# Kernel optimization log

Measured on AMD Instinct MI355X. Metric: run time of the kernel, lower is better.

The kernel has to match this reference:

```python
import jax, jax.numpy as jnp
import numpy as np

N_NODES = 100000
N_EDGES = 600000
N_REL = 4
N_HEADS = 4
DIM = 128  # in_dim == out_dim (required by out = zeros_like(x) + index_add_ of out_dim msgs)
HEAD_DIM = DIM // N_HEADS
NEG_SLOPE = 0.2


def setup_inputs() -> dict:
    key = jax.random.key(0)
    k1, k2, k3, k4, k5 = jax.random.split(key, 5)
    x = jax.random.normal(k1, (N_NODES, DIM), dtype=jnp.float32)
    edge_index = jax.random.randint(k2, (2, N_EDGES), 0, N_NODES, dtype=jnp.int64)
    edge_types = jax.random.randint(k3, (N_EDGES,), 0, N_REL, dtype=jnp.int64)
    # per-relation linear weights, xavier-ish scale
    W = jax.random.normal(k4, (N_REL, DIM, DIM), dtype=jnp.float32) * (1.0 / np.sqrt(DIM))
    # attention vectors [R, H, 2*head_dim]
    attn = jax.random.normal(k5, (N_REL, N_HEADS, 2 * HEAD_DIM), dtype=jnp.float32) * 0.1
    return {"x": x, "edge_index": edge_index, "edge_types": edge_types, "W": W, "attn": attn}


def reference(x, edge_index, edge_types, W, attn):
    N = x.shape[0]
    R, H, twoD = attn.shape
    D = twoD // 2
    E = edge_types.shape[0]

    # per-relation linear transform: [R, N, H, D]
    x_rel = jnp.einsum('ni,rio->rno', x, W).reshape(R, N, H, D)

    src, dst = edge_index[0], edge_index[1]

    # gather per-edge features with the edge's relation
    src_feat = x_rel[edge_types, src]            # [E, H, D]
    dst_feat = x_rel[edge_types, dst]            # [E, H, D]
    a = attn[edge_types]                         # [E, H, 2D]

    # attention logits + LeakyReLU(0.2)
    cat = jnp.concatenate([src_feat, dst_feat], axis=-1)  # [E, H, 2D]
    alpha = jnp.sum(cat * a, axis=-1)                     # [E, H]
    alpha = jnp.where(alpha > 0, alpha, NEG_SLOPE * alpha)

    # segment softmax over edges sharing (relation, dst)
    seg = edge_types * N + dst                            # [E]
    S = R * N
    m = jax.ops.segment_max(alpha, seg, num_segments=S)   # [S, H]
    alpha_exp = jnp.exp(alpha - m[seg])
    denom = jax.ops.segment_sum(alpha_exp, seg, num_segments=S)
    w = alpha_exp / denom[seg]                            # [E, H]

    # weighted messages, scatter-add to dst
    msg = (src_feat * w[..., None]).reshape(E, H * D)     # [E, out_dim]
    out = jax.ops.segment_sum(msg, dst, num_segments=N)   # [N, out_dim]
    return out
```

## Files before the change

### kernel.cpp

```cpp
#include <hip/hip_runtime.h>
#include <hip/hip_bf16.h>
#include <stdint.h>

#define N_NODES 100000
#define N_EDGES 600000
#define N_REL 4
#define N_HEADS 4
#define DIM 128
#define HEAD_DIM 32
#define NEG_SLOPE 0.2f

typedef unsigned int uint;
typedef unsigned short ushort;
typedef __attribute__((ext_vector_type(8))) short bf16x8;
typedef __attribute__((ext_vector_type(4))) float f32x4;

__device__ __forceinline__ float bf2f(ushort u) { return __uint_as_float(((uint)u) << 16); }
__device__ __forceinline__ float lo2f(uint u) { return __uint_as_float(u << 16); }
__device__ __forceinline__ float hi2f(uint u) { return __uint_as_float(u & 0xffff0000u); }
__device__ __forceinline__ ushort f2bf(float f) {
    uint u = __float_as_uint(f);
    uint r = (u + 0x7fffu + ((u >> 16) & 1u)) >> 16;
    return (ushort)r;
}
__device__ __forceinline__ float lrelu(float v) { return v > 0.f ? v : NEG_SLOPE * v; }

__device__ __forceinline__ int bf16_plaus(ushort u) {
    int ex = (u >> 7) & 0xFF;
    return (ex >= 100 && ex <= 140) ? 1 : 0;
}
__global__ void k_detect(const ushort* __restrict__ x, const ushort* __restrict__ W,
                         const ushort* __restrict__ attn, const int* __restrict__ ei,
                         const int* __restrict__ et, int* __restrict__ flags) {
    __shared__ int cnt[5];
    int t = threadIdx.x;
    if (t < 5) cnt[t] = 0;
    __syncthreads();
    if (t < 128) {
        atomicAdd(&cnt[0], bf16_plaus(x[2 * t]));
        atomicAdd(&cnt[1], bf16_plaus(W[2 * t]));
        atomicAdd(&cnt[2], bf16_plaus(attn[2 * t]));
        atomicAdd(&cnt[3], (ei[2 * t + 1] != 0) ? 1 : 0);
        atomicAdd(&cnt[4], (et[2 * t + 1] != 0) ? 1 : 0);
    }
    __syncthreads();
    if (t == 0) {
        flags[0] = (cnt[0] < 64) ? 1 : 0;
        flags[1] = (cnt[1] < 64) ? 1 : 0;
        flags[2] = (cnt[2] < 64) ? 1 : 0;
        flags[3] = (cnt[3] < 8) ? 1 : 0;
        flags[4] = (cnt[4] < 8) ? 1 : 0;
    }
}

__global__ __launch_bounds__(256) void k_canon_i(
    const int* __restrict__ src, int* __restrict__ dst, int n,
    const int* __restrict__ flags, int flagIdx) {
    int i0 = (blockIdx.x * 256 + threadIdx.x) * 4;
    int i64f = flags[flagIdx];
#pragma unroll
    for (int j = 0; j < 4; j++) {
        int i = i0 + j;
        if (i < n) dst[i] = i64f ? src[2 * i] : src[i];
    }
}

__global__ __launch_bounds__(256) void k_cvt_x(
    const void* __restrict__ xv, const int* __restrict__ flags,
    ushort* __restrict__ x_bf)
{
    int t = blockIdx.x * 256 + threadIdx.x;
    if (t >= N_NODES * DIM / 8) return;
    if (flags[0]) {
        const float4* p = (const float4*)xv + (size_t)t * 2;
        float4 f0 = p[0], f1 = p[1];
        uint4 o;
        o.x = (uint)f2bf(f0.x) | ((uint)f2bf(f0.y) << 16);
        o.y = (uint)f2bf(f0.z) | ((uint)f2bf(f0.w) << 16);
        o.z = (uint)f2bf(f1.x) | ((uint)f2bf(f1.y) << 16);
        o.w = (uint)f2bf(f1.z) | ((uint)f2bf(f1.w) << 16);
        ((uint4*)x_bf)[t] = o;
    } else {
        ((uint4*)x_bf)[t] = ((const uint4*)xv)[t];
    }
}

__global__ __launch_bounds__(256) void k_prep_w(
    const void* __restrict__ Wv, const void* __restrict__ av,
    const int* __restrict__ flags,
    ushort* __restrict__ Wt_g, ushort* __restrict__ at_g)
{
    __shared__ ushort wt[128][136];
    const int r = blockIdx.x;
    const int tid = threadIdx.x;
    const int wf = flags[1], af = flags[2];

    if (wf) {
        const float4* Wg = (const float4*)((const float*)Wv + (size_t)r * DIM * DIM);
        for (int it = 0; it < 16; ++it) {
            int idx = tid + it * 256;
            int k = idx >> 5, n4 = (idx & 31) * 4;
            float4 v = Wg[idx];
            wt[n4 + 0][k] = f2bf(v.x);
            wt[n4 + 1][k] = f2bf(v.y);
            wt[n4 + 2][k] = f2bf(v.z);
            wt[n4 + 3][k] = f2bf(v.w);
        }
    } else {
        const ushort* Wg = (const ushort*)Wv + (size_t)r * DIM * DIM;
        for (int it = 0; it < 16; ++it) {
            int idx = tid + it * 256;
            int k = idx >> 5, n4 = (idx & 31) * 4;
            const ushort* p = Wg + (size_t)k * DIM + n4;
            wt[n4 + 0][k] = p[0];
            wt[n4 + 1][k] = p[1];
            wt[n4 + 2][k] = p[2];
            wt[n4 + 3][k] = p[3];
        }
    }
    __syncthreads();

    for (int it = 0; it < 9; ++it) {
        int idx = tid + it * 256;
        if (idx < 2176) {
            int row = idx / 17, c8 = (idx % 17) * 8;
            *(uint4*)(Wt_g + ((size_t)r * 128 + row) * 136 + c8) = *(const uint4*)&wt[row][c8];
        }
    }
    for (int it = 0; it < 9; ++it) {
        int idx = tid + it * 256;
        if (idx < 16 * 136) {
            int n = idx / 136, k = idx % 136;
            int h = n & 3, sd = (n >> 2) & 1;
            float v = 0.f;
            if (n < 8 && k < 128) {
                int d = k - h * 32;
                if (d >= 0 && d < 32) {
                    size_t ai = ((size_t)(r * N_HEADS + h)) * 64 + (size_t)sd * 32 + d;
                    v = af ? ((const float*)av)[ai] : bf2f(((const ushort*)av)[ai]);
                }
            }
            at_g[((size_t)r * 16 + n) * 136 + k] = f2bf(v);
        }
    }
}

__global__ __launch_bounds__(256) void k_gemm_mfma(
    const ushort* __restrict__ x_bf, const ushort* __restrict__ Wt_g,
    const ushort* __restrict__ at_g,
    ushort* __restrict__ x_rel, float* __restrict__ sTab)
{
    __shared__ ushort wt[128][136];
    __shared__ ushort at[16][136];

    const int tid = threadIdx.x;
    const int wave = tid >> 6, lane = tid & 63;
    const int quad = lane >> 4, l16 = lane & 15;
    const int r = blockIdx.x & 3;
    const int n0 = (blockIdx.x >> 2) * 128;

    {
        const uint4* src  = (const uint4*)(Wt_g + (size_t)r * 128 * 136);
        const uint4* srcA = (const uint4*)(at_g + (size_t)r * 16 * 136);
        uint4* dstL = (uint4*)&wt[0][0];
        uint4* dstA = (uint4*)&at[0][0];
#pragma unroll
        for (int it = 0; it < 10; ++it) {
            int idx = tid + it * 256;
            if (idx < 2176) dstL[idx] = src[idx];
            else if (idx < 2448) dstA[idx - 2176] = srcA[idx - 2176];
        }
    }

    const int rowA0 = n0 + wave * 32 + l16;
    const int rowA1 = rowA0 + 16;
    const size_t rA0 = (size_t)min(rowA0, N_NODES - 1) * DIM;
    const size_t rA1 = (size_t)min(rowA1, N_NODES - 1) * DIM;

    __syncthreads();

    f32x4 acc[2][8];
#pragma unroll
    for (int rt = 0; rt < 2; ++rt)
#pragma unroll
        for (int ct = 0; ct < 8; ++ct) acc[rt][ct] = (f32x4){0.f, 0.f, 0.f, 0.f};

#pragma unroll
    for (int q = 0; q < 4; ++q) {
        const int kb = q * 32 + quad * 8;
        bf16x8 a0 = *(const bf16x8*)(x_bf + rA0 + kb);
        bf16x8 a1 = *(const bf16x8*)(x_bf + rA1 + kb);
#pragma unroll
        for (int ct = 0; ct < 8; ++ct) {
            bf16x8 b = *(const bf16x8*)&wt[ct * 16 + l16][kb];
            acc[0][ct] = __builtin_amdgcn_mfma_f32_16x16x32_bf16(a0, b, acc[0][ct], 0, 0, 0);
            acc[1][ct] = __builtin_amdgcn_mfma_f32_16x16x32_bf16(a1, b, acc[1][ct], 0, 0, 0);
        }
    }
    __syncthreads();

    {
        ushort* rp = &wt[0][0];
#pragma unroll
        for (int rt = 0; rt < 2; ++rt) {
            int rowb = wave * 32 + rt * 16 + quad * 4;
#pragma unroll
            for (int ct = 0; ct < 8; ++ct) {
                int col = ct * 16 + l16;
#pragma unroll
                for (int reg = 0; reg < 4; ++reg)
                    rp[(rowb + reg) * 136 + col] = f2bf(acc[rt][ct][reg]);
            }
        }
    }
    __syncthreads();

    {
        const ushort* rp = &wt[0][0];
        f32x4 sacc[2];
        sacc[0] = (f32x4){0.f, 0.f, 0.f, 0.f};
        sacc[1] = (f32x4){0.f, 0.f, 0.f, 0.f};
#pragma unroll
        for (int q = 0; q < 4; ++q) {
            const int kb = q * 32 + quad * 8;
            bf16x8 a0 = *(const bf16x8*)(rp + (wave * 32 + l16) * 136 + kb);
            bf16x8 a1 = *(const bf16x8*)(rp + (wave * 32 + 16 + l16) * 136 + kb);
            bf16x8 bat = *(const bf16x8*)&at[l16][kb];
            sacc[0] = __builtin_amdgcn_mfma_f32_16x16x32_bf16(a0, bat, sacc[0], 0, 0, 0);
            sacc[1] = __builtin_amdgcn_mfma_f32_16x16x32_bf16(a1, bat, sacc[1], 0, 0, 0);
        }
        if (l16 < 8) {
#pragma unroll
            for (int rt = 0; rt < 2; ++rt) {
#pragma unroll
                for (int reg = 0; reg < 4; ++reg) {
                    int node = n0 + wave * 32 + rt * 16 + quad * 4 + reg;
                    if (node < N_NODES)
                        sTab[((size_t)r * N_NODES + node) * 8 + l16] = sacc[rt][reg];
                }
            }
        }
    }

    {
        const ushort* rp = &wt[0][0];
        const size_t rbase = (size_t)r * N_NODES * DIM;
#pragma unroll
        for (int p = 0; p < 8; ++p) {
            int row = p * 16 + (tid >> 4);
            int chunk = tid & 15;
            int node = n0 + row;
            if (node < N_NODES) {
                uint4 v = *(const uint4*)(rp + row * 136 + chunk * 8);
                *(uint4*)(x_rel + rbase + (size_t)node * DIM + chunk * 8) = v;
            }
        }
    }
}

__global__ __launch_bounds__(256) void k_hist(
    const int* __restrict__ ei, uint* __restrict__ deg)
{
    int e = blockIdx.x * 256 + threadIdx.x;
    if (e >= N_EDGES) return;
    atomicAdd(&deg[ei[N_EDGES + e]], 1u);
}

__global__ __launch_bounds__(256) void k_scan1(
    const uint* __restrict__ deg, uint* __restrict__ excl, uint* __restrict__ bsum)
{
    __shared__ uint tmp[256];
    int i = blockIdx.x * 256 + threadIdx.x;
    uint v = (i < N_NODES) ? deg[i] : 0u;
    tmp[threadIdx.x] = v;
    __syncthreads();
    for (int off = 1; off < 256; off <<= 1) {
        uint t = (threadIdx.x >= off) ? tmp[threadIdx.x - off] : 0u;
        __syncthreads();
        tmp[threadIdx.x] += t;
        __syncthreads();
    }
    if (i < N_NODES) excl[i] = tmp[threadIdx.x] - v;
    if (threadIdx.x == 255) bsum[blockIdx.x] = tmp[255];
}

__global__ __launch_bounds__(512) void k_scan2(uint* __restrict__ bsum, int nblocks)
{
    __shared__ uint tmp[512];
    int t = threadIdx.x;
    uint v = (t < nblocks) ? bsum[t] : 0u;
    tmp[t] = v;
    __syncthreads();
    for (int off = 1; off < 512; off <<= 1) {
        uint tt = (t >= off) ? tmp[t - off] : 0u;
        __syncthreads();
        tmp[t] += tt;
        __syncthreads();
    }
    if (t < nblocks) bsum[t] = tmp[t] - v;
}

__global__ __launch_bounds__(256) void k_scan3(
    const uint* __restrict__ excl, const uint* __restrict__ bsum,
    uint* __restrict__ start, uint* __restrict__ cursor)
{
    int i = blockIdx.x * 256 + threadIdx.x;
    if (i >= N_NODES) return;
    uint s = excl[i] + bsum[blockIdx.x];
    start[i] = s;
    cursor[i] = s;
}

__global__ __launch_bounds__(256) void k_fill(
    const int* __restrict__ ei, const int* __restrict__ et,
    uint* __restrict__ cursor, uint* __restrict__ csrPack)
{
    int e = blockIdx.x * 256 + threadIdx.x;
    if (e >= N_EDGES) return;
    int s = ei[e];
    int d = ei[N_EDGES + e];
    int r = et[e];
    uint pos = atomicAdd(&cursor[d], 1u);
    csrPack[pos] = (uint)s | ((uint)r << 27);
}

__device__ __forceinline__ void edge_exp(
    const uint* __restrict__ csrPack, const float* __restrict__ sTab,
    uint st, int m, int lane, int dst,
    uint& pk, float& x0, float& x1, float& x2, float& x3)
{
    pk = 0; x0 = 0.f; x1 = 0.f; x2 = 0.f; x3 = 0.f;
    if (lane < m) {
        pk = csrPack[st + lane];
        int re = (int)(pk >> 27);
        uint s = pk & 0x07FFFFFFu;
        float4 a = *(const float4*)(sTab + ((size_t)re * N_NODES + s) * 8);
        float4 b = *(const float4*)(sTab + ((size_t)re * N_NODES + dst) * 8 + 4);
        x0 = __expf(lrelu(a.x + b.x));
        x1 = __expf(lrelu(a.y + b.y));
        x2 = __expf(lrelu(a.z + b.z));
        x3 = __expf(lrelu(a.w + b.w));
    }
}

__global__ __launch_bounds__(256) void k_gather_fused(
    const uint* __restrict__ start, const uint* __restrict__ deg,
    const uint* __restrict__ csrPack, const float* __restrict__ sTab,
    const uint* __restrict__ x_rel_u, float* __restrict__ out)
{
    const int wv = threadIdx.x >> 6;
    const int dst = blockIdx.x * 4 + wv;
    if (dst >= N_NODES) return;
    const int lane = threadIdx.x & 63;
    const int h = lane >> 4;

    const uint st = start[dst];
    const uint dg = deg[dst];
    float a0 = 0.f, a1 = 0.f;

    if (dg != 0u && dg <= 64u) {
        const int m = (int)dg;
        uint pk; float x0, x1, x2, x3;
        edge_exp(csrPack, sTab, st, m, lane, dst, pk, x0, x1, x2, x3);

        float s0 = 0.f, s1 = 0.f, s2 = 0.f, s3 = 0.f;
        for (int e = 0; e < m; ++e) {
            uint pkE = __shfl(pk, e);
            float y0 = __shfl(x0, e), y1 = __shfl(x1, e);
            float y2 = __shfl(x2, e), y3 = __shfl(x3, e);
            float yh = (h < 2) ? (h == 0 ? y0 : y1) : (h == 2 ? y2 : y3);
            int reE = (int)(pkE >> 27);
            s0 += (reE == 0) ? yh : 0.f;
            s1 += (reE == 1) ? yh : 0.f;
            s2 += (reE == 2) ? yh : 0.f;
            s3 += (reE == 3) ? yh : 0.f;
        }
        float r0 = 1.f / s0, r1 = 1.f / s1, r2 = 1.f / s2, r3 = 1.f / s3;

        for (int e = 0; e < m; ++e) {
            uint pkE = __shfl(pk, e);
            float y0 = __shfl(x0, e), y1 = __shfl(x1, e);
            float y2 = __shfl(x2, e), y3 = __shfl(x3, e);
            float yh = (h < 2) ? (h == 0 ? y0 : y1) : (h == 2 ? y2 : y3);
            int reE = (int)(pkE >> 27);
            float rs = (reE < 2) ? (reE == 0 ? r0 : r1) : (reE == 2 ? r2 : r3);
            float mw = yh * rs;
            uint s = pkE & 0x07FFFFFFu;
            uint u = x_rel_u[((size_t)(pkE >> 27) * N_NODES + s) * 64 + lane];
            a0 = fmaf(mw, lo2f(u), a0);
            a1 = fmaf(mw, hi2f(u), a1);
        }
    } else if (dg > 64u) {
        float s0 = 0.f, s1 = 0.f, s2 = 0.f, s3 = 0.f;
        for (uint c0 = 0; c0 < dg; c0 += 64) {
            int m = (int)min(64u, dg - c0);
            uint pk; float x0, x1, x2, x3;
            edge_exp(csrPack, sTab, st + c0, m, lane, dst, pk, x0, x1, x2, x3);
            for (int e = 0; e < m; ++e) {
                uint pkE = __shfl(pk, e);
                float y0 = __shfl(x0, e), y1 = __shfl(x1, e);
                float y2 = __shfl(x2, e), y3 = __shfl(x3, e);
                float yh = (h < 2) ? (h == 0 ? y0 : y1) : (h == 2 ? y2 : y3);
                int reE = (int)(pkE >> 27);
                s0 += (reE == 0) ? yh : 0.f;
                s1 += (reE == 1) ? yh : 0.f;
                s2 += (reE == 2) ? yh : 0.f;
                s3 += (reE == 3) ? yh : 0.f;
            }
        }
        float r0 = 1.f / s0, r1 = 1.f / s1, r2 = 1.f / s2, r3 = 1.f / s3;
        for (uint c0 = 0; c0 < dg; c0 += 64) {
            int m = (int)min(64u, dg - c0);
            uint pk; float x0, x1, x2, x3;
            edge_exp(csrPack, sTab, st + c0, m, lane, dst, pk, x0, x1, x2, x3);
            for (int e = 0; e < m; ++e) {
                uint pkE = __shfl(pk, e);
                float y0 = __shfl(x0, e), y1 = __shfl(x1, e);
                float y2 = __shfl(x2, e), y3 = __shfl(x3, e);
                float yh = (h < 2) ? (h == 0 ? y0 : y1) : (h == 2 ? y2 : y3);
                int reE = (int)(pkE >> 27);
                float rs = (reE < 2) ? (reE == 0 ? r0 : r1) : (reE == 2 ? r2 : r3);
                float mw = yh * rs;
                uint s = pkE & 0x07FFFFFFu;
                uint u = x_rel_u[((size_t)(pkE >> 27) * N_NODES + s) * 64 + lane];
                a0 = fmaf(mw, lo2f(u), a0);
                a1 = fmaf(mw, hi2f(u), a1);
            }
        }
    }
    float* ob = out + (size_t)dst * DIM + lane * 2;
    ob[0] = a0;
    ob[1] = a1;
}

extern "C" void kernel_launch(void* const* d_in, const int* in_sizes, int n_in,
                              void* d_out, int out_size, void* d_ws, size_t ws_size,
                              hipStream_t stream) {
    const void* x    = d_in[0];
    const int*  ei   = (const int*)d_in[1];
    const int*  et   = (const int*)d_in[2];
    const void* W    = d_in[3];
    const void* attn = d_in[4];
    float* out = (float*)d_out;

    char* ws = (char*)d_ws;
    int*    flags   = (int*)(ws + 0);
    int*    eic     = (int*)(ws + 256);
    int*    etc_    = (int*)(ws + 4800256);
    float*  sTab    = (float*)(ws + 7200256);
    ushort* x_rel   = (ushort*)(ws + 20000256);
    uint*   deg     = (uint*)(ws + 122400256);
    uint*   excl    = (uint*)(ws + 122800256);
    uint*   bsum    = (uint*)(ws + 123200256);
    uint*   startA  = (uint*)(ws + 123202304);
    uint*   cursor  = (uint*)(ws + 123602304);
    uint*   csrPack = (uint*)(ws + 124002304);
    ushort* x_bf    = (ushort*)(ws + 126402304);
    ushort* Wt_g    = (ushort*)(ws + 122800256);
    ushort* at_g    = (ushort*)(ws + 123202304);

    const int NBLK = (N_NODES + 255) / 256;

    hipMemsetAsync(deg, 0, 400000, stream);

    k_detect<<<1, 256, 0, stream>>>((const ushort*)x, (const ushort*)W,
                                    (const ushort*)attn, ei, et, flags);
    k_prep_w<<<N_REL, 256, 0, stream>>>(W, attn, flags, Wt_g, at_g);
    k_canon_i<<<(2 * N_EDGES / 4 + 255) / 256, 256, 0, stream>>>(ei, eic, 2 * N_EDGES, flags, 3);
    k_canon_i<<<(N_EDGES / 4 + 255) / 256, 256, 0, stream>>>(et, etc_, N_EDGES, flags, 4);
    k_cvt_x<<<(N_NODES * DIM / 8 + 255) / 256, 256, 0, stream>>>(x, flags, x_bf);

    k_gemm_mfma<<<((N_NODES + 127) / 128) * N_REL, 256, 0, stream>>>(x_bf, Wt_g, at_g,
                                                                     x_rel, sTab);

    k_hist<<<(N_EDGES + 255) / 256, 256, 0, stream>>>(eic, deg);
    k_scan1<<<NBLK, 256, 0, stream>>>(deg, excl, bsum);
    k_scan2<<<1, 512, 0, stream>>>(bsum, NBLK);
    k_scan3<<<NBLK, 256, 0, stream>>>(excl, bsum, startA, cursor);
    k_fill<<<(N_EDGES + 255) / 256, 256, 0, stream>>>(eic, etc_, cursor, csrPack);
    k_gather_fused<<<(N_NODES + 3) / 4, 256, 0, stream>>>(startA, deg, csrPack, sTab,
                                                          (const uint*)x_rel, out);
}
```

Before: 325.3 us.

## Split softmax weight computation into a per-node kernel before the gather

Softmax weight computation moves out of the wavefront-per-node gather kernel into a new thread-per-node kernel. It computes per-relation denominators and writes normalized per-edge, per-head weights to a workspace table that reuses the x_bf buffer. The gather then only streams csrPack, the weights and x_rel rows, dropping the shuffle-based two-pass loops. This trades an extra launch, an extra weight-table write and read, and a serial per-thread edge loop with little parallelism for a simpler, less divergent gather.

```diff
diff --git a/kernel.cpp b/kernel.cpp
--- a/kernel.cpp
+++ b/kernel.cpp
@@ -324,28 +324,68 @@
     csrPack[pos] = (uint)s | ((uint)r << 27);
 }
 
-__device__ __forceinline__ void edge_exp(
+__global__ __launch_bounds__(256) void k_weights(
+    const uint* __restrict__ start, const uint* __restrict__ deg,
     const uint* __restrict__ csrPack, const float* __restrict__ sTab,
-    uint st, int m, int lane, int dst,
-    uint& pk, float& x0, float& x1, float& x2, float& x3)
-{
-    pk = 0; x0 = 0.f; x1 = 0.f; x2 = 0.f; x3 = 0.f;
-    if (lane < m) {
-        pk = csrPack[st + lane];
+    float* __restrict__ wTab)
+{
+    int d = blockIdx.x * 256 + threadIdx.x;
+    if (d >= N_NODES) return;
+    const uint st = start[d];
+    const uint dg = deg[d];
+    if (dg == 0u) return;
+
+    float4 bp0 = *(const float4*)(sTab + ((size_t)0 * N_NODES + d) * 8 + 4);
+    float4 bp1 = *(const float4*)(sTab + ((size_t)1 * N_NODES + d) * 8 + 4);
+    float4 bp2 = *(const float4*)(sTab + ((size_t)2 * N_NODES + d) * 8 + 4);
+    float4 bp3 = *(const float4*)(sTab + ((size_t)3 * N_NODES + d) * 8 + 4);
+
+    float4 dn0 = {0.f, 0.f, 0.f, 0.f}, dn1 = dn0, dn2 = dn0, dn3 = dn0;
+
+    for (uint e = 0; e < dg; ++e) {
+        uint pk = csrPack[st + e];
         int re = (int)(pk >> 27);
         uint s = pk & 0x07FFFFFFu;
         float4 a = *(const float4*)(sTab + ((size_t)re * N_NODES + s) * 8);
-        float4 b = *(const float4*)(sTab + ((size_t)re * N_NODES + dst) * 8 + 4);
-        x0 = __expf(lrelu(a.x + b.x));
-        x1 = __expf(lrelu(a.y + b.y));
-        x2 = __expf(lrelu(a.z + b.z));
-        x3 = __expf(lrelu(a.w + b.w));
-    }
-}
-
-__global__ __launch_bounds__(256) void k_gather_fused(
+        float4 bp = (re < 2) ? (re == 0 ? bp0 : bp1) : (re == 2 ? bp2 : bp3);
+        float y0 = __expf(lrelu(a.x + bp.x));
+        float y1 = __expf(lrelu(a.y + bp.y));
+        float y2 = __expf(lrelu(a.z + bp.z));
+        float y3 = __expf(lrelu(a.w + bp.w));
+        dn0.x += (re == 0) ? y0 : 0.f;  dn0.y += (re == 0) ? y1 : 0.f;
+        dn0.z += (re == 0) ? y2 : 0.f;  dn0.w += (re == 0) ? y3 : 0.f;
+        dn1.x += (re == 1) ? y0 : 0.f;  dn1.y += (re == 1) ? y1 : 0.f;
+        dn1.z += (re == 1) ? y2 : 0.f;  dn1.w += (re == 1) ? y3 : 0.f;
+        dn2.x += (re == 2) ? y0 : 0.f;  dn2.y += (re == 2) ? y1 : 0.f;
+        dn2.z += (re == 2) ? y2 : 0.f;  dn2.w += (re == 2) ? y3 : 0.f;
+        dn3.x += (re == 3) ? y0 : 0.f;  dn3.y += (re == 3) ? y1 : 0.f;
+        dn3.z += (re == 3) ? y2 : 0.f;  dn3.w += (re == 3) ? y3 : 0.f;
+    }
+    float4 rd0, rd1, rd2, rd3;
+    rd0.x = 1.f / dn0.x; rd0.y = 1.f / dn0.y; rd0.z = 1.f / dn0.z; rd0.w = 1.f / dn0.w;
+    rd1.x = 1.f / dn1.x; rd1.y = 1.f / dn1.y; rd1.z = 1.f / dn1.z; rd1.w = 1.f / dn1.w;
+    rd2.x = 1.f / dn2.x; rd2.y = 1.f / dn2.y; rd2.z = 1.f / dn2.z; rd2.w = 1.f / dn2.w;
+    rd3.x = 1.f / dn3.x; rd3.y = 1.f / dn3.y; rd3.z = 1.f / dn3.z; rd3.w = 1.f / dn3.w;
+
+    for (uint e = 0; e < dg; ++e) {
+        uint pk = csrPack[st + e];
+        int re = (int)(pk >> 27);
+        uint s = pk & 0x07FFFFFFu;
+        float4 a = *(const float4*)(sTab + ((size_t)re * N_NODES + s) * 8);
+        float4 bp = (re < 2) ? (re == 0 ? bp0 : bp1) : (re == 2 ? bp2 : bp3);
+        float4 rs = (re < 2) ? (re == 0 ? rd0 : rd1) : (re == 2 ? rd2 : rd3);
+        float4 w;
+        w.x = __expf(lrelu(a.x + bp.x)) * rs.x;
+        w.y = __expf(lrelu(a.y + bp.y)) * rs.y;
+        w.z = __expf(lrelu(a.z + bp.z)) * rs.z;
+        w.w = __expf(lrelu(a.w + bp.w)) * rs.w;
+        ((float4*)wTab)[st + e] = w;
+    }
+}
+
+__global__ __launch_bounds__(256) void k_gather2(
     const uint* __restrict__ start, const uint* __restrict__ deg,
-    const uint* __restrict__ csrPack, const float* __restrict__ sTab,
+    const uint* __restrict__ csrPack, const float* __restrict__ wTab,
     const uint* __restrict__ x_rel_u, float* __restrict__ out)
 {
     const int wv = threadIdx.x >> 6;
@@ -358,79 +398,17 @@
     const uint dg = deg[dst];
     float a0 = 0.f, a1 = 0.f;
 
-    if (dg != 0u && dg <= 64u) {
-        const int m = (int)dg;
-        uint pk; float x0, x1, x2, x3;
-        edge_exp(csrPack, sTab, st, m, lane, dst, pk, x0, x1, x2, x3);
-
-        float s0 = 0.f, s1 = 0.f, s2 = 0.f, s3 = 0.f;
-        for (int e = 0; e < m; ++e) {
-            uint pkE = __shfl(pk, e);
-            float y0 = __shfl(x0, e), y1 = __shfl(x1, e);
-            float y2 = __shfl(x2, e), y3 = __shfl(x3, e);
-            float yh = (h < 2) ? (h == 0 ? y0 : y1) : (h == 2 ? y2 : y3);
-            int reE = (int)(pkE >> 27);
-            s0 += (reE == 0) ? yh : 0.f;
-            s1 += (reE == 1) ? yh : 0.f;
-            s2 += (reE == 2) ? yh : 0.f;
-            s3 += (reE == 3) ? yh : 0.f;
-        }
-        float r0 = 1.f / s0, r1 = 1.f / s1, r2 = 1.f / s2, r3 = 1.f / s3;
-
-        for (int e = 0; e < m; ++e) {
-            uint pkE = __shfl(pk, e);
-            float y0 = __shfl(x0, e), y1 = __shfl(x1, e);
-            float y2 = __shfl(x2, e), y3 = __shfl(x3, e);
-            float yh = (h < 2) ? (h == 0 ? y0 : y1) : (h == 2 ? y2 : y3);
-            int reE = (int)(pkE >> 27);
-            float rs = (reE < 2) ? (reE == 0 ? r0 : r1) : (reE == 2 ? r2 : r3);
-            float mw = yh * rs;
-            uint s = pkE & 0x07FFFFFFu;
-            uint u = x_rel_u[((size_t)(pkE >> 27) * N_NODES + s) * 64 + lane];
-            a0 = fmaf(mw, lo2f(u), a0);
-            a1 = fmaf(mw, hi2f(u), a1);
-        }
-    } else if (dg > 64u) {
-        float s0 = 0.f, s1 = 0.f, s2 = 0.f, s3 = 0.f;
-        for (uint c0 = 0; c0 < dg; c0 += 64) {
-            int m = (int)min(64u, dg - c0);
-            uint pk; float x0, x1, x2, x3;
-            edge_exp(csrPack, sTab, st + c0, m, lane, dst, pk, x0, x1, x2, x3);
-            for (int e = 0; e < m; ++e) {
-                uint pkE = __shfl(pk, e);
-                float y0 = __shfl(x0, e), y1 = __shfl(x1, e);
-                float y2 = __shfl(x2, e), y3 = __shfl(x3, e);
-                float yh = (h < 2) ? (h == 0 ? y0 : y1) : (h == 2 ? y2 : y3);
-                int reE = (int)(pkE >> 27);
-                s0 += (reE == 0) ? yh : 0.f;
-                s1 += (reE == 1) ? yh : 0.f;
-                s2 += (reE == 2) ? yh : 0.f;
-                s3 += (reE == 3) ? yh : 0.f;
-            }
-        }
-        float r0 = 1.f / s0, r1 = 1.f / s1, r2 = 1.f / s2, r3 = 1.f / s3;
-        for (uint c0 = 0; c0 < dg; c0 += 64) {
-            int m = (int)min(64u, dg - c0);
-            uint pk; float x0, x1, x2, x3;
-            edge_exp(csrPack, sTab, st + c0, m, lane, dst, pk, x0, x1, x2, x3);
-            for (int e = 0; e < m; ++e) {
-                uint pkE = __shfl(pk, e);
-                float y0 = __shfl(x0, e), y1 = __shfl(x1, e);
-                float y2 = __shfl(x2, e), y3 = __shfl(x3, e);
-                float yh = (h < 2) ? (h == 0 ? y0 : y1) : (h == 2 ? y2 : y3);
-                int reE = (int)(pkE >> 27);
-                float rs = (reE < 2) ? (reE == 0 ? r0 : r1) : (reE == 2 ? r2 : r3);
-                float mw = yh * rs;
-                uint s = pkE & 0x07FFFFFFu;
-                uint u = x_rel_u[((size_t)(pkE >> 27) * N_NODES + s) * 64 + lane];
-                a0 = fmaf(mw, lo2f(u), a0);
-                a1 = fmaf(mw, hi2f(u), a1);
-            }
-        }
-    }
-    float* ob = out + (size_t)dst * DIM + lane * 2;
-    ob[0] = a0;
-    ob[1] = a1;
+    for (uint e = 0; e < dg; ++e) {
+        uint pk = csrPack[st + e];
+        float mw = wTab[(size_t)(st + e) * 4 + h];
+        uint s = pk & 0x07FFFFFFu;
+        uint re = pk >> 27;
+        uint u = x_rel_u[((size_t)re * N_NODES + s) * 64 + lane];
+        a0 = fmaf(mw, lo2f(u), a0);
+        a1 = fmaf(mw, hi2f(u), a1);
+    }
+    float2 o; o.x = a0; o.y = a1;
+    *(float2*)(out + (size_t)dst * DIM + lane * 2) = o;
 }
 
 extern "C" void kernel_launch(void* const* d_in, const int* in_sizes, int n_in,
@@ -458,6 +436,7 @@
     ushort* x_bf    = (ushort*)(ws + 126402304);
     ushort* Wt_g    = (ushort*)(ws + 122800256);
     ushort* at_g    = (ushort*)(ws + 123202304);
+    float*  wTab    = (float*)(ws + 126402304);
 
     const int NBLK = (N_NODES + 255) / 256;
 
@@ -478,6 +457,7 @@
     k_scan2<<<1, 512, 0, stream>>>(bsum, NBLK);
     k_scan3<<<NBLK, 256, 0, stream>>>(excl, bsum, startA, cursor);
     k_fill<<<(N_EDGES + 255) / 256, 256, 0, stream>>>(eic, etc_, cursor, csrPack);
-    k_gather_fused<<<(N_NODES + 3) / 4, 256, 0, stream>>>(startA, deg, csrPack, sTab,
-                                                          (const uint*)x_rel, out);
-}
+    k_weights<<<NBLK, 256, 0, stream>>>(startA, deg, csrPack, sTab, wTab);
+    k_gather2<<<(N_NODES + 3) / 4, 256, 0, stream>>>(startA, deg, csrPack, wTab,
+                                                     (const uint*)x_rel, out);
+}
```

Result: slower. 358.6 us (+10.2%).
